# Kernel optimization log

Hardware: AMD Instinct MI355X
Metric: run time of the kernel (lower is better)

Reference implementation:

```python
import jax, jax.numpy as jnp
import numpy as np

B, P, COV, H, S = 1024, 96, 31, 1024, 100  # batch, pred_len, cov_dim, hidden, num_samples
IN = COV + 1


def setup_inputs() -> dict:
    key = jax.random.key(0)
    ks = jax.random.split(key, 16)
    sc = 1.0 / np.sqrt(H)
    return {
        "covariates": jax.random.normal(ks[0], (B, P, COV), jnp.float32),
        "initial_value": jax.random.normal(ks[1], (B, 1), jnp.float32),
        "noise": jax.random.normal(ks[2], (P, S, B), jnp.float32),
        "h_init": jax.random.normal(ks[3], (2, B, H), jnp.float32) * 0.1,
        "c_init": jax.random.normal(ks[4], (2, B, H), jnp.float32) * 0.1,
        "W_ih0": jax.random.normal(ks[5], (4 * H, IN), jnp.float32) * sc,
        "W_hh0": jax.random.normal(ks[6], (4 * H, H), jnp.float32) * sc,
        "b_ih0": jax.random.normal(ks[7], (4 * H,), jnp.float32) * sc,
        "b_hh0": jax.random.normal(ks[8], (4 * H,), jnp.float32) * sc,
        "W_ih1": jax.random.normal(ks[9], (4 * H, H), jnp.float32) * sc,
        "W_hh1": jax.random.normal(ks[10], (4 * H, H), jnp.float32) * sc,
        "b_ih1": jax.random.normal(ks[11], (4 * H,), jnp.float32) * sc,
        "b_hh1": jax.random.normal(ks[12], (4 * H,), jnp.float32) * sc,
        "W_proj": jax.random.normal(ks[13], (2, H), jnp.float32) * sc,
        "b_proj": jax.random.normal(ks[14], (2,), jnp.float32) * sc,
    }


def _lstm_cell(x, h, c, W_ih, W_hh, b_ih, b_hh):
    # PyTorch gate order: i, f, g, o
    gates = x @ W_ih.T + h @ W_hh.T + b_ih + b_hh  # [B, 4H]
    i, f, g, o = jnp.split(gates, 4, axis=-1)
    i, f, o = jax.nn.sigmoid(i), jax.nn.sigmoid(f), jax.nn.sigmoid(o)
    g = jnp.tanh(g)
    c_new = f * c + i * g
    h_new = o * jnp.tanh(c_new)
    return h_new, c_new


def reference(covariates, initial_value, noise, h_init, c_init,
              W_ih0, W_hh0, b_ih0, b_hh0, W_ih1, W_hh1, b_ih1, b_hh1,
              W_proj, b_proj):
    def step(carry, inp):
        h0, c0, h1, c1, cur = carry
        cov_t, noise_t = inp  # [B, COV], [S, B]
        x = jnp.concatenate([cur[:, None], cov_t], axis=-1)  # [B, IN]
        h0, c0 = _lstm_cell(x, h0, c0, W_ih0, W_hh0, b_ih0, b_hh0)
        h1, c1 = _lstm_cell(h0, h1, c1, W_ih1, W_hh1, b_ih1, b_hh1)
        params = h1 @ W_proj.T + b_proj  # [B, 2]
        mu = params[:, 0]
        sigma = jax.nn.softplus(params[:, 1]) + 1e-6
        samples = mu[None, :] + sigma[None, :] * noise_t  # [S, B]
        cur = samples[0]
        return (h0, c0, h1, c1, cur), (params, samples)

    carry0 = (h_init[0], c_init[0], h_init[1], c_init[1], initial_value[:, 0])
    xs = (jnp.swapaxes(covariates, 0, 1), noise)  # time-major
    _, (all_params, all_samples) = jax.lax.scan(step, carry0, xs)
    all_params = jnp.swapaxes(all_params, 0, 1)       # [B, P, 2]
    all_samples = jnp.transpose(all_samples, (1, 2, 0))  # [S, B, P]
    return all_params, all_samples
```

## Files before the change

kernel.cpp:

```cpp
#include <hip/hip_runtime.h>
#include <stdint.h>

#define Bsz 1024
#define Hsz 1024
#define Psteps 96
#define Ssamp 100
#define COVn 31

typedef __attribute__((ext_vector_type(8))) short short8;
typedef __attribute__((ext_vector_type(4))) float f32x4;

__device__ inline unsigned short f2bf(float f) {
    union { float f; unsigned u; } v; v.f = f;
    unsigned r = v.u + 0x7FFFu + ((v.u >> 16) & 1u);
    return (unsigned short)(r >> 16);
}

__device__ inline float sigm(float x) { return 1.f / (1.f + __expf(-x)); }
__device__ inline float tanh_f(float x) { return 2.f / (1.f + __expf(-2.f * x)) - 1.f; }
__device__ inline float softplusf(float x) {
    return fmaxf(x, 0.f) + log1pf(__expf(-fabsf(x)));
}

__device__ inline void gld16(const unsigned short* g, unsigned short* l) {
    auto gp = (const __attribute__((address_space(1))) unsigned int*)(const unsigned int*)g;
    auto lp = (__attribute__((address_space(3))) unsigned int*)(unsigned int*)l;
    __builtin_amdgcn_global_load_lds(gp, lp, 16, 0, 0);
}

template<int CH>
__device__ inline void stage_tile(const unsigned short* __restrict__ src, int rowStride,
                                  int row0, int k0, unsigned short* ldsBase, int tid) {
    #pragma unroll
    for (int i = 0; i < CH; ++i) {
        int c = i * 256 + tid;
        int row = c >> 3, s = c & 7;
        int col = ((s ^ (row & 7)) << 3) + k0;
        gld16(src + (size_t)(row0 + row) * rowStride + col, ldsBase + c * 8);
    }
}

__global__ void prep_weights(const float* __restrict__ Wih0, const float* __restrict__ Whh0,
                             const float* __restrict__ Wih1, const float* __restrict__ Whh1,
                             const float* __restrict__ bih0, const float* __restrict__ bhh0,
                             const float* __restrict__ bih1, const float* __restrict__ bhh1,
                             unsigned short* __restrict__ W0cat, unsigned short* __restrict__ W1cat,
                             float* __restrict__ bias0, float* __restrict__ bias1) {
    const size_t N0 = (size_t)4096 * 1088;
    const size_t N1 = (size_t)4096 * 2048;
    const size_t total = N0 + N1 + 8192;
    for (size_t e = (size_t)blockIdx.x * 256 + threadIdx.x; e < total; e += (size_t)gridDim.x * 256) {
        if (e < N0) {
            int gh = (int)(e / 1088), col = (int)(e % 1088);
            int src = ((gh & 3) << 10) + (gh >> 2);
            float v;
            if (col < 32) v = Wih0[(size_t)src * 32 + col];
            else if (col < 64) v = 0.f;
            else v = Whh0[(size_t)src * 1024 + (col - 64)];
            W0cat[e] = f2bf(v);
        } else if (e < N0 + N1) {
            size_t m = e - N0;
            int gh = (int)(m >> 11), col = (int)(m & 2047);
            int src = ((gh & 3) << 10) + (gh >> 2);
            float v = (col < 1024) ? Wih1[(size_t)src * 1024 + col]
                                   : Whh1[(size_t)src * 1024 + (col - 1024)];
            W1cat[m] = f2bf(v);
        } else {
            size_t m = e - N0 - N1;
            int which = (int)(m >> 12);
            int gh = (int)(m & 4095);
            int src = ((gh & 3) << 10) + (gh >> 2);
            if (which == 0) bias0[gh] = bih0[src] + bhh0[src];
            else            bias1[gh] = bih1[src] + bhh1[src];
        }
    }
}

__global__ void prep_state(const float* __restrict__ hinit, const float* __restrict__ cinit,
                           unsigned short* __restrict__ hb0, unsigned short* __restrict__ hb1,
                           float* __restrict__ c0, float* __restrict__ c1) {
    const size_t NM = (size_t)1024 * 1024;
    for (size_t e = (size_t)blockIdx.x * 256 + threadIdx.x; e < 4 * NM; e += (size_t)gridDim.x * 256) {
        if (e < NM) {
            hb0[e] = f2bf(hinit[e]);
        } else if (e < 2 * NM) {
            hb1[e - NM] = f2bf(hinit[e]);
        } else if (e < 3 * NM) {
            size_t j = e - 2 * NM; int h = (int)(j >> 10), b = (int)(j & 1023);
            c0[j] = cinit[(size_t)b * 1024 + h];
        } else {
            size_t j = e - 3 * NM; int h = (int)(j >> 10), b = (int)(j & 1023);
            c1[j] = cinit[NM + (size_t)b * 1024 + h];
        }
    }
}

template<int CELL>
__global__ __launch_bounds__(256, 2) void lstm_step(
        int t,
        const float* __restrict__ cov, const float* __restrict__ initv,
        const float* __restrict__ noise, const float* __restrict__ bproj,
        const float* __restrict__ wproj,
        const unsigned short* __restrict__ WA,
        const float* __restrict__ biasH,
        const unsigned short* __restrict__ hA,
        const unsigned short* __restrict__ hB,
        unsigned short* __restrict__ hOut,
        float* __restrict__ cws,
        float* __restrict__ pbufPartial,
        float* __restrict__ outParams) {
    __shared__ __align__(16) char smem[49152];

    const int tid = threadIdx.x;
    const int m_tile = blockIdx.x & 31;
    const int n_tile = blockIdx.x >> 5;
    const int m0 = m_tile * 128;
    const int hc0 = m_tile * 32;
    const int b0 = n_tile * 64;
    const int lane = tid & 63;
    const int wid = tid >> 6;
    const int wm = wid >> 1, wn = wid & 1;
    const int NIT = (CELL == 0) ? 17 : 32;

    auto stageIt = [&](int j) {
        unsigned short* Ab = (unsigned short*)(smem + (j & 1) * 16384);
        unsigned short* Bb = (unsigned short*)(smem + 32768 + (j & 1) * 8192);
        if (CELL == 0) {
            stage_tile<4>(WA, 1088, m0, j * 64, Ab, tid);
            if (j > 0) stage_tile<2>(hB, 1024, b0, (j - 1) * 64, Bb, tid);
        } else {
            stage_tile<4>(WA, 2048, m0, j * 64, Ab, tid);
            if (j < 16) stage_tile<2>(hA, 1024, b0, j * 64, Bb, tid);
            else        stage_tile<2>(hB, 1024, b0, (j - 16) * 64, Bb, tid);
        }
    };

    stageIt(0);
    if (CELL == 0) {
        float* pj = (float*)(smem + 40960);
        float* curF = (float*)(smem + 40960 + 512);
        if (t > 0) {
            if (tid < 128) {
                int bl = tid >> 1, j = tid & 1;
                float s = bproj[j];
                #pragma unroll 8
                for (int m = 0; m < 32; ++m)
                    s += pbufPartial[(size_t)((m << 10) + b0 + bl) * 2 + j];
                pj[tid] = s;
                if (m_tile == 0)
                    outParams[((size_t)(b0 + bl) * Psteps + (t - 1)) * 2 + j] = s;
            }
        }
        __syncthreads();
        if (tid < 64) {
            float cu;
            if (t == 0) {
                cu = initv[b0 + tid];
            } else {
                float p0 = pj[tid * 2 + 0], p1 = pj[tid * 2 + 1];
                cu = p0 + (softplusf(p1) + 1e-6f) * noise[(size_t)(t - 1) * (Ssamp * Bsz) + b0 + tid];
            }
            curF[tid] = cu;
        }
        __syncthreads();
        #pragma unroll
        for (int i = 0; i < 2; ++i) {
            int c = i * 256 + tid;
            int row = c >> 3, s = c & 7;
            int ts = s ^ (row & 7);
            short8 v;
            if (ts < 4) {
                const float* cr = cov + ((size_t)(b0 + row) * Psteps + t) * COVn;
                #pragma unroll
                for (int e = 0; e < 8; ++e) {
                    int col = ts * 8 + e;
                    float x = (col == 0) ? curF[row] : cr[col - 1];
                    v[e] = (short)f2bf(x);
                }
            } else {
                v = (short8){0, 0, 0, 0, 0, 0, 0, 0};
            }
            *(short8*)(smem + 32768 + c * 16) = v;
        }
    }
    __syncthreads();

    f32x4 acc[4][2];
    #pragma unroll
    for (int i = 0; i < 4; ++i)
        #pragma unroll
        for (int j = 0; j < 2; ++j) acc[i][j] = (f32x4){0.f, 0.f, 0.f, 0.f};

    for (int it = 0; it < NIT; ++it) {
        if (it + 1 < NIT) stageIt(it + 1);
        const char* Abuf = smem + (it & 1) * 16384;
        const char* Bbuf = smem + 32768 + (it & 1) * 8192;
        __builtin_amdgcn_s_setprio(1);
        #pragma unroll
        for (int kh = 0; kh < 2; ++kh) {
            short8 af[4], bq[2];
            #pragma unroll
            for (int mf = 0; mf < 4; ++mf) {
                int row = wm * 64 + mf * 16 + (lane & 15);
                int slot = (kh * 4 + (lane >> 4)) ^ (row & 7);
                af[mf] = *(const short8*)(Abuf + row * 128 + slot * 16);
            }
            #pragma unroll
            for (int nf = 0; nf < 2; ++nf) {
                int row = wn * 32 + nf * 16 + (lane & 15);
                int slot = (kh * 4 + (lane >> 4)) ^ (row & 7);
                bq[nf] = *(const short8*)(Bbuf + row * 128 + slot * 16);
            }
            #pragma unroll
            for (int mf = 0; mf < 4; ++mf)
                #pragma unroll
                for (int nf = 0; nf < 2; ++nf)
                    acc[mf][nf] = __builtin_amdgcn_mfma_f32_16x16x32_bf16(af[mf], bq[nf], acc[mf][nf], 0, 0, 0);
        }
        __builtin_amdgcn_s_setprio(0);
        __syncthreads();
    }

    unsigned short* Ht = (unsigned short*)smem;
    float* part = (float*)(smem + 16384);
    float pp[2][2];
    if (CELL == 1) {
        #pragma unroll
        for (int nf = 0; nf < 2; ++nf) { pp[nf][0] = 0.f; pp[nf][1] = 0.f; }
    }
    #pragma unroll
    for (int mf = 0; mf < 4; ++mf) {
        int hl = wm * 16 + mf * 4 + (lane >> 4);
        int h = hc0 + hl;
        f32x4 bs = *(const f32x4*)&biasH[h * 4];
        #pragma unroll
        for (int nf = 0; nf < 2; ++nf) {
            int bl = wn * 32 + nf * 16 + (lane & 15);
            int b = b0 + bl;
            f32x4 v = acc[mf][nf];
            float gi = sigm(v.x + bs.x);
            float gf = sigm(v.y + bs.y);
            float gg = tanh_f(v.z + bs.z);
            float go = sigm(v.w + bs.w);
            size_t ci = (size_t)h * Bsz + b;
            float cn = gf * cws[ci] + gi * gg;
            cws[ci] = cn;
            float hn = go * tanh_f(cn);
            Ht[bl * 40 + hl] = f2bf(hn);
            if (CELL == 1) {
                pp[nf][0] += hn * wproj[h];
                pp[nf][1] += hn * wproj[Hsz + h];
            }
        }
    }
    if (CELL == 1) {
        #pragma unroll
        for (int nf = 0; nf < 2; ++nf)
            #pragma unroll
            for (int j = 0; j < 2; ++j) {
                float v = pp[nf][j];
                v += __shfl_xor(v, 16, 64);
                v += __shfl_xor(v, 32, 64);
                if (lane < 16)
                    part[((wm * 64) + wn * 32 + nf * 16 + lane) * 2 + j] = v;
            }
    }
    __syncthreads();
    if (tid < 128) {
        int row = tid >> 1, hf = tid & 1;
        short8 v0 = *(const short8*)&Ht[row * 40 + hf * 16];
        short8 v1 = *(const short8*)&Ht[row * 40 + hf * 16 + 8];
        *(short8*)&hOut[(size_t)(b0 + row) * Hsz + hc0 + hf * 16] = v0;
        *(short8*)&hOut[(size_t)(b0 + row) * Hsz + hc0 + hf * 16 + 8] = v1;
    }
    if (CELL == 1 && tid < 128) {
        int bl = tid >> 1, j = tid & 1;
        pbufPartial[((size_t)m_tile * 1024 + b0 + bl) * 2 + j] =
            part[bl * 2 + j] + part[(64 + bl) * 2 + j];
    }
}

__global__ void tail_params(const float* __restrict__ pPart, const float* __restrict__ bproj,
                            float* __restrict__ dout, float* __restrict__ musig) {
    int idx = blockIdx.x * 256 + threadIdx.x;
    if (idx >= Bsz * Psteps) return;
    int b = idx / Psteps, t = idx % Psteps;
    float p0, p1;
    if (t == Psteps - 1) {
        p0 = bproj[0]; p1 = bproj[1];
        #pragma unroll 8
        for (int m = 0; m < 32; ++m) {
            p0 += pPart[(size_t)((m << 10) + b) * 2 + 0];
            p1 += pPart[(size_t)((m << 10) + b) * 2 + 1];
        }
        dout[(size_t)idx * 2 + 0] = p0;
        dout[(size_t)idx * 2 + 1] = p1;
    } else {
        p0 = dout[(size_t)idx * 2 + 0];
        p1 = dout[(size_t)idx * 2 + 1];
    }
    musig[(size_t)idx * 2 + 0] = p0;
    musig[(size_t)idx * 2 + 1] = softplusf(p1) + 1e-6f;
}

__global__ __launch_bounds__(256) void gen_samples(const float* __restrict__ noise,
                                                   const float* __restrict__ musig,
                                                   float* __restrict__ outS) {
    __shared__ float tile[16][97];
    int s = blockIdx.x >> 6;
    int b0 = (blockIdx.x & 63) << 4;
    int tid = threadIdx.x;
    for (int e = tid; e < Psteps * 16; e += 256) {
        int tt = e >> 4, b = e & 15;
        tile[b][tt] = noise[((size_t)tt * Ssamp + s) * Bsz + b0 + b];
    }
    __syncthreads();
    int b = tid >> 4, t0 = (tid & 15) * 6;
    const float* ms = musig + ((size_t)(b0 + b) * Psteps + t0) * 2;
    float* op = outS + ((size_t)s * Bsz + b0 + b) * Psteps + t0;
    #pragma unroll
    for (int k = 0; k < 6; ++k) {
        op[k] = ms[k * 2] + ms[k * 2 + 1] * tile[b][t0 + k];
    }
}

extern "C" void kernel_launch(void* const* d_in, const int* in_sizes, int n_in,
                              void* d_out, int out_size, void* d_ws, size_t ws_size,
                              hipStream_t stream) {
    const float* cov   = (const float*)d_in[0];
    const float* initv = (const float*)d_in[1];
    const float* noise = (const float*)d_in[2];
    const float* hinit = (const float*)d_in[3];
    const float* cinit = (const float*)d_in[4];
    const float* Wih0  = (const float*)d_in[5];
    const float* Whh0  = (const float*)d_in[6];
    const float* bih0  = (const float*)d_in[7];
    const float* bhh0  = (const float*)d_in[8];
    const float* Wih1  = (const float*)d_in[9];
    const float* Whh1  = (const float*)d_in[10];
    const float* bih1  = (const float*)d_in[11];
    const float* bih1x = bih1;
    const float* bhh1  = (const float*)d_in[12];
    const float* wproj = (const float*)d_in[13];
    const float* bproj = (const float*)d_in[14];
    (void)bih1x;
    float* dout = (float*)d_out;

    uint8_t* p = (uint8_t*)d_ws;
    auto alloc = [&](size_t bytes) { void* r = (void*)p; p += (bytes + 255) & ~(size_t)255; return r; };
    unsigned short* W0cat = (unsigned short*)alloc((size_t)4096 * 1088 * 2);
    unsigned short* W1cat = (unsigned short*)alloc((size_t)4096 * 2048 * 2);
    float* bias0 = (float*)alloc(4096 * 4);
    float* bias1 = (float*)alloc(4096 * 4);
    unsigned short* hb0 = (unsigned short*)alloc((size_t)2 * 1024 * 1024 * 2 + 256);
    unsigned short* hb1 = (unsigned short*)alloc((size_t)2 * 1024 * 1024 * 2 + 256);
    float* c0 = (float*)alloc((size_t)1024 * 1024 * 4);
    float* c1 = (float*)alloc((size_t)1024 * 1024 * 4);
    float* pbufPartial = (float*)alloc((size_t)32 * 1024 * 2 * 4);
    float* musig = (float*)alloc((size_t)1024 * 96 * 2 * 4);

    prep_weights<<<2048, 256, 0, stream>>>(Wih0, Whh0, Wih1, Whh1, bih0, bhh0, bih1, bhh1,
                                           W0cat, W1cat, bias0, bias1);
    prep_state<<<2048, 256, 0, stream>>>(hinit, cinit, hb0, hb1, c0, c1);

    const size_t HB = (size_t)1024 * 1024;
    for (int t = 0; t < Psteps; ++t) {
        const unsigned short* h0p = hb0 + (size_t)(t & 1) * HB;
        unsigned short* h0n = hb0 + (size_t)((t + 1) & 1) * HB;
        const unsigned short* h1p = hb1 + (size_t)(t & 1) * HB;
        unsigned short* h1n = hb1 + (size_t)((t + 1) & 1) * HB;
        lstm_step<0><<<512, 256, 0, stream>>>(t, cov, initv, noise, bproj, wproj,
                                              W0cat, bias0, nullptr, h0p, h0n, c0,
                                              pbufPartial, dout);
        lstm_step<1><<<512, 256, 0, stream>>>(t, cov, initv, noise, bproj, wproj,
                                              W1cat, bias1, h0n, h1p, h1n, c1,
                                              pbufPartial, dout);
    }
    tail_params<<<384, 256, 0, stream>>>(pbufPartial, bproj, dout, musig);
    gen_samples<<<6400, 256, 0, stream>>>(noise, musig, dout + (size_t)Bsz * Psteps * 2);
}
```

Measured before the change: 4.068 ms.

## Prefetch hidden-state tiles into registers two iterations ahead with manual waitcnt

Hidden-state (B operand) tiles are no longer loaded straight into LDS. They are now read into registers two K-iterations ahead and written into the alternate LDS buffer after each compute step. Weight tiles still use direct global-to-LDS loads. The per-iteration __syncthreads is replaced by explicit s_waitcnt vmcnt(2) plus s_barrier, with scheduling barriers, so the in-flight register prefetch does not block the barrier. This aims to hide global latency of the activation loads behind MFMA work, at the cost of more VGPRs and fragile hand-written wait counts.

Result: slower. 5.141 ms (+26.4%).

```diff
diff --git a/kernel.cpp b/kernel.cpp
--- a/kernel.cpp
+++ b/kernel.cpp
@@ -9,6 +9,7 @@
 
 typedef __attribute__((ext_vector_type(8))) short short8;
 typedef __attribute__((ext_vector_type(4))) float f32x4;
+typedef __attribute__((ext_vector_type(4))) unsigned int u32x4;
 
 __device__ inline unsigned short f2bf(float f) {
     union { float f; unsigned u; } v; v.f = f;
@@ -26,18 +27,6 @@
     auto gp = (const __attribute__((address_space(1))) unsigned int*)(const unsigned int*)g;
     auto lp = (__attribute__((address_space(3))) unsigned int*)(unsigned int*)l;
     __builtin_amdgcn_global_load_lds(gp, lp, 16, 0, 0);
-}
-
-template<int CH>
-__device__ inline void stage_tile(const unsigned short* __restrict__ src, int rowStride,
-                                  int row0, int k0, unsigned short* ldsBase, int tid) {
-    #pragma unroll
-    for (int i = 0; i < CH; ++i) {
-        int c = i * 256 + tid;
-        int row = c >> 3, s = c & 7;
-        int col = ((s ^ (row & 7)) << 3) + k0;
-        gld16(src + (size_t)(row0 + row) * rowStride + col, ldsBase + c * 8);
-    }
 }
 
 __global__ void prep_weights(const float* __restrict__ Wih0, const float* __restrict__ Whh0,
@@ -121,23 +110,69 @@
     const int wid = tid >> 6;
     const int wm = wid >> 1, wn = wid & 1;
     const int NIT = (CELL == 0) ? 17 : 32;
-
-    auto stageIt = [&](int j) {
-        unsigned short* Ab = (unsigned short*)(smem + (j & 1) * 16384);
-        unsigned short* Bb = (unsigned short*)(smem + 32768 + (j & 1) * 8192);
-        if (CELL == 0) {
-            stage_tile<4>(WA, 1088, m0, j * 64, Ab, tid);
-            if (j > 0) stage_tile<2>(hB, 1024, b0, (j - 1) * 64, Bb, tid);
-        } else {
-            stage_tile<4>(WA, 2048, m0, j * 64, Ab, tid);
-            if (j < 16) stage_tile<2>(hA, 1024, b0, j * 64, Bb, tid);
-            else        stage_tile<2>(hB, 1024, b0, (j - 16) * 64, Bb, tid);
+    const int Wstride = (CELL == 0) ? 1088 : 2048;
+
+    const int br0 = tid >> 3;
+    const int br1 = 32 + br0;
+    const int bs0 = ((tid & 7) ^ (br0 & 7)) << 3;
+
+    auto stageA = [&](int k0, int bufsel) {
+        unsigned short* Ab = (unsigned short*)(smem + bufsel * 16384);
+        #pragma unroll
+        for (int i = 0; i < 4; ++i) {
+            int c = i * 256 + tid;
+            int row = c >> 3, s = c & 7;
+            int col = ((s ^ (row & 7)) << 3) + k0;
+            gld16(WA + (size_t)(m0 + row) * Wstride + col, Ab + c * 8);
         }
     };
-
-    stageIt(0);
+    auto bAddr = [&](int it) -> const unsigned short* {
+        if (CELL == 0) return hB + (it - 1) * 64;
+        if (it < 16)   return hA + it * 64;
+        return hB + (it - 16) * 64;
+    };
+    auto bLoad = [&](int it, u32x4& a, u32x4& b) {
+        const unsigned short* h = bAddr(it);
+        a = *(const u32x4*)(h + (size_t)(b0 + br0) * 1024 + bs0);
+        b = *(const u32x4*)(h + (size_t)(b0 + br1) * 1024 + bs0);
+    };
+    auto bCommit = [&](int bufsel, const u32x4& a, const u32x4& b) {
+        char* Bb = smem + 32768 + bufsel * 8192;
+        *(u32x4*)(Bb + tid * 16) = a;
+        *(u32x4*)(Bb + 4096 + tid * 16) = b;
+    };
+    auto computeIter = [&](int bufsel, f32x4 (&acc)[4][2]) {
+        const char* Abuf = smem + bufsel * 16384;
+        const char* Bbuf = smem + 32768 + bufsel * 8192;
+        __builtin_amdgcn_s_setprio(1);
+        #pragma unroll
+        for (int kh = 0; kh < 2; ++kh) {
+            short8 af[4], bq[2];
+            #pragma unroll
+            for (int mf = 0; mf < 4; ++mf) {
+                int row = wm * 64 + mf * 16 + (lane & 15);
+                int slot = (kh * 4 + (lane >> 4)) ^ (row & 7);
+                af[mf] = *(const short8*)(Abuf + row * 128 + slot * 16);
+            }
+            #pragma unroll
+            for (int nf = 0; nf < 2; ++nf) {
+                int row = wn * 32 + nf * 16 + (lane & 15);
+                int slot = (kh * 4 + (lane >> 4)) ^ (row & 7);
+                bq[nf] = *(const short8*)(Bbuf + row * 128 + slot * 16);
+            }
+            #pragma unroll
+            for (int mf = 0; mf < 4; ++mf)
+                #pragma unroll
+                for (int nf = 0; nf < 2; ++nf)
+                    acc[mf][nf] = __builtin_amdgcn_mfma_f32_16x16x32_bf16(af[mf], bq[nf], acc[mf][nf], 0, 0, 0);
+        }
+        __builtin_amdgcn_s_setprio(0);
+    };
+
+    u32x4 sE0, sE1, sO0, sO1;
+    stageA(0, 0);
     if (CELL == 0) {
-        float* pj = (float*)(smem + 40960);
+        float* pj   = (float*)(smem + 40960);
         float* curF = (float*)(smem + 40960 + 512);
         if (t > 0) {
             if (tid < 128) {
@@ -182,7 +217,11 @@
             }
             *(short8*)(smem + 32768 + c * 16) = v;
         }
-    }
+    } else {
+        bLoad(0, sE0, sE1);
+        bCommit(0, sE0, sE1);
+    }
+    bLoad(1, sO0, sO1);
     __syncthreads();
 
     f32x4 acc[4][2];
@@ -192,33 +231,24 @@
         for (int j = 0; j < 2; ++j) acc[i][j] = (f32x4){0.f, 0.f, 0.f, 0.f};
 
     for (int it = 0; it < NIT; ++it) {
-        if (it + 1 < NIT) stageIt(it + 1);
-        const char* Abuf = smem + (it & 1) * 16384;
-        const char* Bbuf = smem + 32768 + (it & 1) * 8192;
-        __builtin_amdgcn_s_setprio(1);
-        #pragma unroll
-        for (int kh = 0; kh < 2; ++kh) {
-            short8 af[4], bq[2];
-            #pragma unroll
-            for (int mf = 0; mf < 4; ++mf) {
-                int row = wm * 64 + mf * 16 + (lane & 15);
-                int slot = (kh * 4 + (lane >> 4)) ^ (row & 7);
-                af[mf] = *(const short8*)(Abuf + row * 128 + slot * 16);
-            }
-            #pragma unroll
-            for (int nf = 0; nf < 2; ++nf) {
-                int row = wn * 32 + nf * 16 + (lane & 15);
-                int slot = (kh * 4 + (lane >> 4)) ^ (row & 7);
-                bq[nf] = *(const short8*)(Bbuf + row * 128 + slot * 16);
-            }
-            #pragma unroll
-            for (int mf = 0; mf < 4; ++mf)
-                #pragma unroll
-                for (int nf = 0; nf < 2; ++nf)
-                    acc[mf][nf] = __builtin_amdgcn_mfma_f32_16x16x32_bf16(af[mf], bq[nf], acc[mf][nf], 0, 0, 0);
-        }
-        __builtin_amdgcn_s_setprio(0);
-        __syncthreads();
+        const bool hasC = (it + 1 < NIT);
+        const bool hasI = (it + 2 < NIT);
+        if (hasC) stageA((it + 1) * 64, (it + 1) & 1);
+        __builtin_amdgcn_sched_barrier(0);
+        if (hasI) {
+            if (it & 1) bLoad(it + 2, sO0, sO1);
+            else        bLoad(it + 2, sE0, sE1);
+        }
+        __builtin_amdgcn_sched_barrier(0);
+        computeIter(it & 1, acc);
+        if (hasC) {
+            if (it & 1) bCommit((it + 1) & 1, sE0, sE1);
+            else        bCommit((it + 1) & 1, sO0, sO1);
+        }
+        if (hasI) asm volatile("s_waitcnt vmcnt(2) lgkmcnt(0)" ::: "memory");
+        else      asm volatile("s_waitcnt vmcnt(0) lgkmcnt(0)" ::: "memory");
+        __builtin_amdgcn_s_barrier();
+        __builtin_amdgcn_sched_barrier(0);
     }
 
     unsigned short* Ht = (unsigned short*)smem;
@@ -339,11 +369,9 @@
     const float* Wih1  = (const float*)d_in[9];
     const float* Whh1  = (const float*)d_in[10];
     const float* bih1  = (const float*)d_in[11];
-    const float* bih1x = bih1;
     const float* bhh1  = (const float*)d_in[12];
     const float* wproj = (const float*)d_in[13];
     const float* bproj = (const float*)d_in[14];
-    (void)bih1x;
     float* dout = (float*)d_out;
 
     uint8_t* p = (uint8_t*)d_ws;
```

## Fuse per-step LSTM launches into one persistent kernel with flag sync

Applied to the files above, without the earlier changes.

Replaces the 192 per-timestep kernel launches with a single persistent kernel of 512 blocks. Blocks synchronise through per-step, per-batch-tile atomic flags instead of kernel boundaries. Each block also reorders its work so the recurrent-weight part of each GEMM runs before it waits on the dependency. That overlaps the h-recurrence matmul with the wait for the previous layer and for the projection partials. Correctness now relies on all 512 blocks being co-resident, which launch_bounds(256,2) targets on 256 CUs; if they are not, the spin-waits can deadlock.

Result: slower. 14.50 ms (+256.4%).

```diff
diff --git a/kernel.cpp b/kernel.cpp
--- a/kernel.cpp
+++ b/kernel.cpp
@@ -26,18 +26,6 @@
     auto gp = (const __attribute__((address_space(1))) unsigned int*)(const unsigned int*)g;
     auto lp = (__attribute__((address_space(3))) unsigned int*)(unsigned int*)l;
     __builtin_amdgcn_global_load_lds(gp, lp, 16, 0, 0);
-}
-
-template<int CH>
-__device__ inline void stage_tile(const unsigned short* __restrict__ src, int rowStride,
-                                  int row0, int k0, unsigned short* ldsBase, int tid) {
-    #pragma unroll
-    for (int i = 0; i < CH; ++i) {
-        int c = i * 256 + tid;
-        int row = c >> 3, s = c & 7;
-        int col = ((s ^ (row & 7)) << 3) + k0;
-        gld16(src + (size_t)(row0 + row) * rowStride + col, ldsBase + c * 8);
-    }
 }
 
 __global__ void prep_weights(const float* __restrict__ Wih0, const float* __restrict__ Whh0,
@@ -78,39 +66,39 @@
 
 __global__ void prep_state(const float* __restrict__ hinit, const float* __restrict__ cinit,
                            unsigned short* __restrict__ hb0, unsigned short* __restrict__ hb1,
-                           float* __restrict__ c0, float* __restrict__ c1) {
+                           float* __restrict__ c0, float* __restrict__ c1,
+                           int* __restrict__ flags, int nflags) {
     const size_t NM = (size_t)1024 * 1024;
-    for (size_t e = (size_t)blockIdx.x * 256 + threadIdx.x; e < 4 * NM; e += (size_t)gridDim.x * 256) {
+    const size_t total = 4 * NM + (size_t)nflags;
+    for (size_t e = (size_t)blockIdx.x * 256 + threadIdx.x; e < total; e += (size_t)gridDim.x * 256) {
         if (e < NM) {
-            hb0[e] = f2bf(hinit[e]);
+            hb0[NM + e] = f2bf(hinit[e]);
         } else if (e < 2 * NM) {
-            hb1[e - NM] = f2bf(hinit[e]);
+            hb1[NM + (e - NM)] = f2bf(hinit[e]);
         } else if (e < 3 * NM) {
             size_t j = e - 2 * NM; int h = (int)(j >> 10), b = (int)(j & 1023);
             c0[j] = cinit[(size_t)b * 1024 + h];
-        } else {
+        } else if (e < 4 * NM) {
             size_t j = e - 3 * NM; int h = (int)(j >> 10), b = (int)(j & 1023);
             c1[j] = cinit[NM + (size_t)b * 1024 + h];
-        }
-    }
-}
-
-template<int CELL>
-__global__ __launch_bounds__(256, 2) void lstm_step(
-        int t,
+        } else {
+            flags[e - 4 * NM] = 0;
+        }
+    }
+}
+
+__global__ __launch_bounds__(256, 2) void lstm_persist(
         const float* __restrict__ cov, const float* __restrict__ initv,
         const float* __restrict__ noise, const float* __restrict__ bproj,
         const float* __restrict__ wproj,
-        const unsigned short* __restrict__ WA,
-        const float* __restrict__ biasH,
-        const unsigned short* __restrict__ hA,
-        const unsigned short* __restrict__ hB,
-        unsigned short* __restrict__ hOut,
-        float* __restrict__ cws,
-        float* __restrict__ pbufPartial,
+        const unsigned short* __restrict__ W0, const unsigned short* __restrict__ W1,
+        const float* __restrict__ bias0, const float* __restrict__ bias1,
+        unsigned short* __restrict__ h0buf, unsigned short* __restrict__ h1buf,
+        float* __restrict__ c0, float* __restrict__ c1,
+        float* __restrict__ pPart,
+        int* __restrict__ h0Flag, int* __restrict__ pbFlag,
         float* __restrict__ outParams) {
     __shared__ __align__(16) char smem[49152];
-
     const int tid = threadIdx.x;
     const int m_tile = blockIdx.x & 31;
     const int n_tile = blockIdx.x >> 5;
@@ -120,81 +108,33 @@
     const int lane = tid & 63;
     const int wid = tid >> 6;
     const int wm = wid >> 1, wn = wid & 1;
-    const int NIT = (CELL == 0) ? 17 : 32;
-
-    auto stageIt = [&](int j) {
-        unsigned short* Ab = (unsigned short*)(smem + (j & 1) * 16384);
-        unsigned short* Bb = (unsigned short*)(smem + 32768 + (j & 1) * 8192);
-        if (CELL == 0) {
-            stage_tile<4>(WA, 1088, m0, j * 64, Ab, tid);
-            if (j > 0) stage_tile<2>(hB, 1024, b0, (j - 1) * 64, Bb, tid);
-        } else {
-            stage_tile<4>(WA, 2048, m0, j * 64, Ab, tid);
-            if (j < 16) stage_tile<2>(hA, 1024, b0, j * 64, Bb, tid);
-            else        stage_tile<2>(hB, 1024, b0, (j - 16) * 64, Bb, tid);
-        }
-    };
-
-    stageIt(0);
-    if (CELL == 0) {
-        float* pj = (float*)(smem + 40960);
-        float* curF = (float*)(smem + 40960 + 512);
-        if (t > 0) {
-            if (tid < 128) {
-                int bl = tid >> 1, j = tid & 1;
-                float s = bproj[j];
-                #pragma unroll 8
-                for (int m = 0; m < 32; ++m)
-                    s += pbufPartial[(size_t)((m << 10) + b0 + bl) * 2 + j];
-                pj[tid] = s;
-                if (m_tile == 0)
-                    outParams[((size_t)(b0 + bl) * Psteps + (t - 1)) * 2 + j] = s;
-            }
-        }
-        __syncthreads();
-        if (tid < 64) {
-            float cu;
-            if (t == 0) {
-                cu = initv[b0 + tid];
-            } else {
-                float p0 = pj[tid * 2 + 0], p1 = pj[tid * 2 + 1];
-                cu = p0 + (softplusf(p1) + 1e-6f) * noise[(size_t)(t - 1) * (Ssamp * Bsz) + b0 + tid];
-            }
-            curF[tid] = cu;
-        }
-        __syncthreads();
+    const size_t HB = (size_t)Bsz * Hsz;
+
+    f32x4 acc[4][2];
+
+    auto stageA = [&](const unsigned short* W, int stride, int k0, int bufsel) {
+        unsigned short* Ab = (unsigned short*)(smem + bufsel * 16384);
+        #pragma unroll
+        for (int i = 0; i < 4; ++i) {
+            int c = i * 256 + tid;
+            int row = c >> 3, s = c & 7;
+            int col = ((s ^ (row & 7)) << 3) + k0;
+            gld16(W + (size_t)(m0 + row) * stride + col, Ab + c * 8);
+        }
+    };
+    auto stageB = [&](const unsigned short* hsrc, int k0, int bufsel) {
+        unsigned short* Bb = (unsigned short*)(smem + 32768 + bufsel * 8192);
         #pragma unroll
         for (int i = 0; i < 2; ++i) {
             int c = i * 256 + tid;
             int row = c >> 3, s = c & 7;
-            int ts = s ^ (row & 7);
-            short8 v;
-            if (ts < 4) {
-                const float* cr = cov + ((size_t)(b0 + row) * Psteps + t) * COVn;
-                #pragma unroll
-                for (int e = 0; e < 8; ++e) {
-                    int col = ts * 8 + e;
-                    float x = (col == 0) ? curF[row] : cr[col - 1];
-                    v[e] = (short)f2bf(x);
-                }
-            } else {
-                v = (short8){0, 0, 0, 0, 0, 0, 0, 0};
-            }
-            *(short8*)(smem + 32768 + c * 16) = v;
-        }
-    }
-    __syncthreads();
-
-    f32x4 acc[4][2];
-    #pragma unroll
-    for (int i = 0; i < 4; ++i)
-        #pragma unroll
-        for (int j = 0; j < 2; ++j) acc[i][j] = (f32x4){0.f, 0.f, 0.f, 0.f};
-
-    for (int it = 0; it < NIT; ++it) {
-        if (it + 1 < NIT) stageIt(it + 1);
-        const char* Abuf = smem + (it & 1) * 16384;
-        const char* Bbuf = smem + 32768 + (it & 1) * 8192;
+            int col = ((s ^ (row & 7)) << 3) + k0;
+            gld16(hsrc + (size_t)(b0 + row) * 1024 + col, Bb + c * 8);
+        }
+    };
+    auto computeIter = [&](int bufsel) {
+        const char* Abuf = smem + bufsel * 16384;
+        const char* Bbuf = smem + 32768 + bufsel * 8192;
         __builtin_amdgcn_s_setprio(1);
         #pragma unroll
         for (int kh = 0; kh < 2; ++kh) {
@@ -218,69 +158,200 @@
                     acc[mf][nf] = __builtin_amdgcn_mfma_f32_16x16x32_bf16(af[mf], bq[nf], acc[mf][nf], 0, 0, 0);
         }
         __builtin_amdgcn_s_setprio(0);
+    };
+    auto zeroAcc = [&]() {
+        #pragma unroll
+        for (int i = 0; i < 4; ++i)
+            #pragma unroll
+            for (int j = 0; j < 2; ++j) acc[i][j] = (f32x4){0.f, 0.f, 0.f, 0.f};
+    };
+    auto waitFlag = [&](int* f) {
+        if (tid == 0) {
+            while (__hip_atomic_load(f, __ATOMIC_RELAXED, __HIP_MEMORY_SCOPE_AGENT) < 32)
+                __builtin_amdgcn_s_sleep(8);
+            (void)__hip_atomic_load(f, __ATOMIC_ACQUIRE, __HIP_MEMORY_SCOPE_AGENT);
+        }
         __syncthreads();
-    }
-
-    unsigned short* Ht = (unsigned short*)smem;
-    float* part = (float*)(smem + 16384);
-    float pp[2][2];
-    if (CELL == 1) {
-        #pragma unroll
-        for (int nf = 0; nf < 2; ++nf) { pp[nf][0] = 0.f; pp[nf][1] = 0.f; }
-    }
-    #pragma unroll
-    for (int mf = 0; mf < 4; ++mf) {
-        int hl = wm * 16 + mf * 4 + (lane >> 4);
-        int h = hc0 + hl;
-        f32x4 bs = *(const f32x4*)&biasH[h * 4];
-        #pragma unroll
-        for (int nf = 0; nf < 2; ++nf) {
-            int bl = wn * 32 + nf * 16 + (lane & 15);
-            int b = b0 + bl;
-            f32x4 v = acc[mf][nf];
-            float gi = sigm(v.x + bs.x);
-            float gf = sigm(v.y + bs.y);
-            float gg = tanh_f(v.z + bs.z);
-            float go = sigm(v.w + bs.w);
-            size_t ci = (size_t)h * Bsz + b;
-            float cn = gf * cws[ci] + gi * gg;
-            cws[ci] = cn;
-            float hn = go * tanh_f(cn);
-            Ht[bl * 40 + hl] = f2bf(hn);
-            if (CELL == 1) {
-                pp[nf][0] += hn * wproj[h];
-                pp[nf][1] += hn * wproj[Hsz + h];
-            }
-        }
-    }
-    if (CELL == 1) {
-        #pragma unroll
-        for (int nf = 0; nf < 2; ++nf)
-            #pragma unroll
-            for (int j = 0; j < 2; ++j) {
-                float v = pp[nf][j];
-                v += __shfl_xor(v, 16, 64);
-                v += __shfl_xor(v, 32, 64);
-                if (lane < 16)
-                    part[((wm * 64) + wn * 32 + nf * 16 + lane) * 2 + j] = v;
-            }
-    }
-    __syncthreads();
-    if (tid < 128) {
-        int row = tid >> 1, hf = tid & 1;
-        short8 v0 = *(const short8*)&Ht[row * 40 + hf * 16];
-        short8 v1 = *(const short8*)&Ht[row * 40 + hf * 16 + 8];
-        *(short8*)&hOut[(size_t)(b0 + row) * Hsz + hc0 + hf * 16] = v0;
-        *(short8*)&hOut[(size_t)(b0 + row) * Hsz + hc0 + hf * 16 + 8] = v1;
-    }
-    if (CELL == 1 && tid < 128) {
-        int bl = tid >> 1, j = tid & 1;
-        pbufPartial[((size_t)m_tile * 1024 + b0 + bl) * 2 + j] =
-            part[bl * 2 + j] + part[(64 + bl) * 2 + j];
-    }
-}
-
-__global__ void tail_params(const float* __restrict__ pPart, const float* __restrict__ bproj,
+    };
+    auto signalFlag = [&](int* f) {
+        __syncthreads();
+        if (tid == 0)
+            __hip_atomic_fetch_add(f, 1, __ATOMIC_RELEASE, __HIP_MEMORY_SCOPE_AGENT);
+    };
+
+    for (int t = 0; t < Psteps; ++t) {
+        const int ws = t & 1;
+        const unsigned short* h0r = h0buf + (size_t)(ws ^ 1) * HB;
+        unsigned short*       h0w = h0buf + (size_t)ws * HB;
+        const unsigned short* h1r = h1buf + (size_t)(ws ^ 1) * HB;
+        unsigned short*       h1w = h1buf + (size_t)ws * HB;
+        const float* pRead = pPart + (size_t)(ws ^ 1) * 65536;
+        float*      pWrite = pPart + (size_t)ws * 65536;
+
+        zeroAcc();
+        stageA(W0, 1088, 64, 0);
+        stageB(h0r, 0, 0);
+        __syncthreads();
+        for (int j = 0; j < 16; ++j) {
+            if (j < 15) { stageA(W0, 1088, 64 + (j + 1) * 64, (j + 1) & 1); stageB(h0r, (j + 1) * 64, (j + 1) & 1); }
+            else        { stageA(W0, 1088, 0, 0); }
+            computeIter(j & 1);
+            __syncthreads();
+        }
+        {
+            float* pj   = (float*)(smem + 40960);
+            float* curF = (float*)(smem + 41984);
+            if (t > 0) {
+                waitFlag(&pbFlag[(t - 1) * 16 + n_tile]);
+                if (tid < 128) {
+                    int bl = tid >> 1, jj = tid & 1;
+                    float s = bproj[jj];
+                    #pragma unroll
+                    for (int m = 0; m < 32; ++m)
+                        s += pRead[(size_t)((m << 10) + b0 + bl) * 2 + jj];
+                    pj[tid] = s;
+                    if (m_tile == 0)
+                        outParams[((size_t)(b0 + bl) * Psteps + (t - 1)) * 2 + jj] = s;
+                }
+                __syncthreads();
+            }
+            if (tid < 64) {
+                float cu;
+                if (t == 0) {
+                    cu = initv[b0 + tid];
+                } else {
+                    float p0 = pj[tid * 2 + 0], p1 = pj[tid * 2 + 1];
+                    cu = p0 + (softplusf(p1) + 1e-6f) * noise[(size_t)(t - 1) * (Ssamp * Bsz) + b0 + tid];
+                }
+                curF[tid] = cu;
+            }
+            __syncthreads();
+            #pragma unroll
+            for (int i = 0; i < 2; ++i) {
+                int c = i * 256 + tid;
+                int row = c >> 3, s = c & 7;
+                int ts = s ^ (row & 7);
+                short8 v;
+                if (ts < 4) {
+                    const float* cr = cov + ((size_t)(b0 + row) * Psteps + t) * COVn;
+                    #pragma unroll
+                    for (int e = 0; e < 8; ++e) {
+                        int col = ts * 8 + e;
+                        float x = (col == 0) ? curF[row] : cr[col - 1];
+                        v[e] = (short)f2bf(x);
+                    }
+                } else {
+                    v = (short8){0, 0, 0, 0, 0, 0, 0, 0};
+                }
+                *(short8*)(smem + 32768 + c * 16) = v;
+            }
+            __syncthreads();
+            computeIter(0);
+            __syncthreads();
+        }
+        {
+            unsigned short* Ht = (unsigned short*)smem;
+            #pragma unroll
+            for (int mf = 0; mf < 4; ++mf) {
+                int hl = wm * 16 + mf * 4 + (lane >> 4);
+                int h = hc0 + hl;
+                f32x4 bs = *(const f32x4*)&bias0[h * 4];
+                #pragma unroll
+                for (int nf = 0; nf < 2; ++nf) {
+                    int bl = wn * 32 + nf * 16 + (lane & 15);
+                    f32x4 v = acc[mf][nf];
+                    float gi = sigm(v.x + bs.x);
+                    float gf = sigm(v.y + bs.y);
+                    float gg = tanh_f(v.z + bs.z);
+                    float go = sigm(v.w + bs.w);
+                    size_t ci = (size_t)h * Bsz + b0 + bl;
+                    float cn = gf * c0[ci] + gi * gg;
+                    c0[ci] = cn;
+                    Ht[bl * 40 + hl] = f2bf(go * tanh_f(cn));
+                }
+            }
+            __syncthreads();
+            if (tid < 128) {
+                int row = tid >> 1, hf = tid & 1;
+                short8 v0 = *(const short8*)&Ht[row * 40 + hf * 16];
+                short8 v1 = *(const short8*)&Ht[row * 40 + hf * 16 + 8];
+                *(short8*)&h0w[(size_t)(b0 + row) * Hsz + hc0 + hf * 16] = v0;
+                *(short8*)&h0w[(size_t)(b0 + row) * Hsz + hc0 + hf * 16 + 8] = v1;
+            }
+            signalFlag(&h0Flag[t * 16 + n_tile]);
+        }
+
+        zeroAcc();
+        stageA(W1, 2048, 1024, 0);
+        stageB(h1r, 0, 0);
+        __syncthreads();
+        for (int j = 0; j < 16; ++j) {
+            if (j < 15) { stageA(W1, 2048, 1024 + (j + 1) * 64, (j + 1) & 1); stageB(h1r, (j + 1) * 64, (j + 1) & 1); }
+            else        { stageA(W1, 2048, 0, 0); }
+            computeIter(j & 1);
+            __syncthreads();
+        }
+        waitFlag(&h0Flag[t * 16 + n_tile]);
+        stageB(h0w, 0, 0);
+        __syncthreads();
+        for (int j = 16; j < 32; ++j) {
+            if (j < 31) { stageA(W1, 2048, (j - 15) * 64, (j + 1) & 1); stageB(h0w, (j - 15) * 64, (j + 1) & 1); }
+            computeIter(j & 1);
+            __syncthreads();
+        }
+        {
+            unsigned short* Ht = (unsigned short*)smem;
+            float* part = (float*)(smem + 16384);
+            float pp[2][2] = {{0.f, 0.f}, {0.f, 0.f}};
+            #pragma unroll
+            for (int mf = 0; mf < 4; ++mf) {
+                int hl = wm * 16 + mf * 4 + (lane >> 4);
+                int h = hc0 + hl;
+                f32x4 bs = *(const f32x4*)&bias1[h * 4];
+                #pragma unroll
+                for (int nf = 0; nf < 2; ++nf) {
+                    int bl = wn * 32 + nf * 16 + (lane & 15);
+                    f32x4 v = acc[mf][nf];
+                    float gi = sigm(v.x + bs.x);
+                    float gf = sigm(v.y + bs.y);
+                    float gg = tanh_f(v.z + bs.z);
+                    float go = sigm(v.w + bs.w);
+                    size_t ci = (size_t)h * Bsz + b0 + bl;
+                    float cn = gf * c1[ci] + gi * gg;
+                    c1[ci] = cn;
+                    float hn = go * tanh_f(cn);
+                    Ht[bl * 40 + hl] = f2bf(hn);
+                    pp[nf][0] += hn * wproj[h];
+                    pp[nf][1] += hn * wproj[Hsz + h];
+                }
+            }
+            #pragma unroll
+            for (int nf = 0; nf < 2; ++nf)
+                #pragma unroll
+                for (int j = 0; j < 2; ++j) {
+                    float v = pp[nf][j];
+                    v += __shfl_xor(v, 16, 64);
+                    v += __shfl_xor(v, 32, 64);
+                    if (lane < 16)
+                        part[((wm * 64) + wn * 32 + nf * 16 + lane) * 2 + j] = v;
+                }
+            __syncthreads();
+            if (tid < 128) {
+                int row = tid >> 1, hf = tid & 1;
+                short8 v0 = *(const short8*)&Ht[row * 40 + hf * 16];
+                short8 v1 = *(const short8*)&Ht[row * 40 + hf * 16 + 8];
+                *(short8*)&h1w[(size_t)(b0 + row) * Hsz + hc0 + hf * 16] = v0;
+                *(short8*)&h1w[(size_t)(b0 + row) * Hsz + hc0 + hf * 16 + 8] = v1;
+                int bl = row, jj = hf;
+                pWrite[(size_t)((m_tile << 10) + b0 + bl) * 2 + jj] =
+                    part[bl * 2 + jj] + part[(64 + bl) * 2 + jj];
+            }
+            signalFlag(&pbFlag[t * 16 + n_tile]);
+        }
+    }
+}
+
+__global__ void tail_params(const float* __restrict__ pSlot, const float* __restrict__ bproj,
                             float* __restrict__ dout, float* __restrict__ musig) {
     int idx = blockIdx.x * 256 + threadIdx.x;
     if (idx >= Bsz * Psteps) return;
@@ -290,8 +361,8 @@
         p0 = bproj[0]; p1 = bproj[1];
         #pragma unroll 8
         for (int m = 0; m < 32; ++m) {
-            p0 += pPart[(size_t)((m << 10) + b) * 2 + 0];
-            p1 += pPart[(size_t)((m << 10) + b) * 2 + 1];
+            p0 += pSlot[(size_t)((m << 10) + b) * 2 + 0];
+            p1 += pSlot[(size_t)((m << 10) + b) * 2 + 1];
         }
         dout[(size_t)idx * 2 + 0] = p0;
         dout[(size_t)idx * 2 + 1] = p1;
@@ -339,11 +410,9 @@
     const float* Wih1  = (const float*)d_in[9];
     const float* Whh1  = (const float*)d_in[10];
     const float* bih1  = (const float*)d_in[11];
-    const float* bih1x = bih1;
     const float* bhh1  = (const float*)d_in[12];
     const float* wproj = (const float*)d_in[13];
     const float* bproj = (const float*)d_in[14];
-    (void)bih1x;
     float* dout = (float*)d_out;
 
     uint8_t* p = (uint8_t*)d_ws;
@@ -352,30 +421,25 @@
     unsigned short* W1cat = (unsigned short*)alloc((size_t)4096 * 2048 * 2);
     float* bias0 = (float*)alloc(4096 * 4);
     float* bias1 = (float*)alloc(4096 * 4);
-    unsigned short* hb0 = (unsigned short*)alloc((size_t)2 * 1024 * 1024 * 2 + 256);
-    unsigned short* hb1 = (unsigned short*)alloc((size_t)2 * 1024 * 1024 * 2 + 256);
+    unsigned short* hb0 = (unsigned short*)alloc((size_t)2 * 1024 * 1024 * 2);
+    unsigned short* hb1 = (unsigned short*)alloc((size_t)2 * 1024 * 1024 * 2);
     float* c0 = (float*)alloc((size_t)1024 * 1024 * 4);
     float* c1 = (float*)alloc((size_t)1024 * 1024 * 4);
-    float* pbufPartial = (float*)alloc((size_t)32 * 1024 * 2 * 4);
+    float* pPart = (float*)alloc((size_t)2 * 32 * 1024 * 2 * 4);
     float* musig = (float*)alloc((size_t)1024 * 96 * 2 * 4);
+    int* flags = (int*)alloc((size_t)2 * Psteps * 16 * 4);
+    int* h0Flag = flags;
+    int* pbFlag = flags + Psteps * 16;
+    const int nflags = 2 * Psteps * 16;
 
     prep_weights<<<2048, 256, 0, stream>>>(Wih0, Whh0, Wih1, Whh1, bih0, bhh0, bih1, bhh1,
                                            W0cat, W1cat, bias0, bias1);
-    prep_state<<<2048, 256, 0, stream>>>(hinit, cinit, hb0, hb1, c0, c1);
-
-    const size_t HB = (size_t)1024 * 1024;
-    for (int t = 0; t < Psteps; ++t) {
-        const unsigned short* h0p = hb0 + (size_t)(t & 1) * HB;
-        unsigned short* h0n = hb0 + (size_t)((t + 1) & 1) * HB;
-        const unsigned short* h1p = hb1 + (size_t)(t & 1) * HB;
-        unsigned short* h1n = hb1 + (size_t)((t + 1) & 1) * HB;
-        lstm_step<0><<<512, 256, 0, stream>>>(t, cov, initv, noise, bproj, wproj,
-                                              W0cat, bias0, nullptr, h0p, h0n, c0,
-                                              pbufPartial, dout);
-        lstm_step<1><<<512, 256, 0, stream>>>(t, cov, initv, noise, bproj, wproj,
-                                              W1cat, bias1, h0n, h1p, h1n, c1,
-                                              pbufPartial, dout);
-    }
-    tail_params<<<384, 256, 0, stream>>>(pbufPartial, bproj, dout, musig);
+    prep_state<<<2048, 256, 0, stream>>>(hinit, cinit, hb0, hb1, c0, c1, flags, nflags);
+
+    lstm_persist<<<512, 256, 0, stream>>>(cov, initv, noise, bproj, wproj,
+                                          W0cat, W1cat, bias0, bias1,
+                                          hb0, hb1, c0, c1, pPart, h0Flag, pbFlag, dout);
+
+    tail_params<<<384, 256, 0, stream>>>(pPart + (size_t)((Psteps - 1) & 1) * 65536, bproj, dout, musig);
     gen_samples<<<6400, 256, 0, stream>>>(noise, musig, dout + (size_t)Bsz * Psteps * 2);
 }
```
